# Kernel optimization log

Measured on AMD Instinct MI355X. Metric: run time of the kernel, lower is better.

The kernel has to match this reference:

```python
import jax, jax.numpy as jnp
import numpy as np

NUM_HEADS = 16

def setup_inputs() -> dict:
    key = jax.random.key(0)
    ks = jax.random.split(key, 7)
    B, S, D = 2, 2048, 1024
    X = jax.random.normal(ks[0], (B, S, D), dtype=jnp.float32)
    s = 1.0 / np.sqrt(D)
    Wq = jax.random.normal(ks[1], (D, D), dtype=jnp.float32) * s
    Wk = jax.random.normal(ks[2], (D, D), dtype=jnp.float32) * s
    Wv = jax.random.normal(ks[3], (D, D), dtype=jnp.float32) * s
    Wo = jax.random.normal(ks[4], (D, D), dtype=jnp.float32) * s
    bo = jnp.zeros((D,), dtype=jnp.float32)
    return {"X": X, "Wq": Wq, "Wk": Wk, "Wv": Wv, "Wo": Wo, "bo": bo}

def reference(X, Wq, Wk, Wv, Wo, bo):
    B, S, D = X.shape
    H = NUM_HEADS
    hd = D // H
    # project and split heads -> [B, H, S, hd]
    def split(t):
        return t.reshape(B, S, H, hd).transpose(0, 2, 1, 3)
    q = split(X @ Wq)
    k = split(X @ Wk)
    v = split(X @ Wv)
    scores = jnp.einsum('bhqd,bhkd->bhqk', q, k) / jnp.sqrt(jnp.float32(hd))
    causal = jnp.tril(jnp.ones((S, S), dtype=bool))
    scores = jnp.where(causal, scores, -jnp.inf)
    weights = jax.nn.softmax(scores, axis=-1)  # dropout p=0 -> identity
    ctx = jnp.einsum('bhqk,bhkd->bhqd', weights, v)
    ctx = ctx.transpose(0, 2, 1, 3).reshape(B, S, D)
    return ctx @ Wo + bo
```

## Files before the change

### kernel.cpp

```cpp
#include <hip/hip_runtime.h>


typedef __attribute__((ext_vector_type(8))) short short8;
typedef __attribute__((ext_vector_type(4))) float floatx4;

__device__ inline unsigned short f2bf(float f) {
  unsigned u = __float_as_uint(f);
  unsigned r = (u + 0x7fffu + ((u >> 16) & 1u)) >> 16;
  return (unsigned short)r;
}

__device__ __forceinline__ float fast_exp2(float x) {
#if __has_builtin(__builtin_amdgcn_exp2f)
  return __builtin_amdgcn_exp2f(x);
#else
  float r;
  asm volatile("v_exp_f32_e32 %0, %1" : "=v"(r) : "v"(x));
  return r;
#endif
}

__device__ __forceinline__ void gll16(const unsigned short* g, unsigned short* l) {
  __builtin_amdgcn_global_load_lds(
      (const __attribute__((address_space(1))) unsigned int*)(g),
      (__attribute__((address_space(3))) unsigned int*)(l),
      16, 0, 0);
}

constexpr int B_ = 2, S_ = 2048, D_ = 1024, H_ = 16, HD_ = 64;

__global__ __launch_bounds__(256) void prep_inputs(
    const float* __restrict__ x, unsigned short* __restrict__ xb,
    const float* __restrict__ w0, const float* __restrict__ w1,
    const float* __restrict__ w2, const float* __restrict__ w3,
    unsigned short* __restrict__ wt_base)
{
  if (blockIdx.z == 4) {
    const int tid = threadIdx.y * 32 + threadIdx.x;
    const size_t base =
        ((size_t)(blockIdx.y * 32 + blockIdx.x) * 256 + tid) * 16;
#pragma unroll
    for (int half = 0; half < 2; ++half) {
      const size_t i = base + half * 8;
      float4 a = *(const float4*)(x + i);
      float4 b = *(const float4*)(x + i + 4);
      short8 o;
      o[0] = (short)f2bf(a.x); o[1] = (short)f2bf(a.y);
      o[2] = (short)f2bf(a.z); o[3] = (short)f2bf(a.w);
      o[4] = (short)f2bf(b.x); o[5] = (short)f2bf(b.y);
      o[6] = (short)f2bf(b.z); o[7] = (short)f2bf(b.w);
      *(short8*)(xb + i) = o;
    }
    return;
  }
  const float* src;
  switch (blockIdx.z) {
    case 0: src = w0; break;
    case 1: src = w1; break;
    case 2: src = w2; break;
    default: src = w3; break;
  }
  unsigned short* dst = wt_base + (size_t)blockIdx.z * 1024 * 1024;
  __shared__ unsigned short t[32][33];
  const int bx = blockIdx.x * 32;
  const int by = blockIdx.y * 32;
  const int x_ = threadIdx.x;
  for (int yy = threadIdx.y; yy < 32; yy += 8)
    t[yy][x_] = f2bf(src[(size_t)(by + yy) * 1024 + bx + x_]);
  __syncthreads();
  for (int yy = threadIdx.y; yy < 32; yy += 8)
    dst[(size_t)(bx + yy) * 1024 + by + x_] = t[x_][yy];
}

__global__ __launch_bounds__(256) void transpose_v(
    const unsigned short* __restrict__ Vb, unsigned short* __restrict__ Vt)
{
  __shared__ unsigned short t[32][33];
  const int bh = blockIdx.z;
  const int b = bh >> 4, h = bh & 15;
  const int s0 = blockIdx.x * 32, d0 = blockIdx.y * 32;
  const int x = threadIdx.x;
  for (int yy = threadIdx.y; yy < 32; yy += 8)
    t[yy][x] = Vb[(size_t)(b * 2048 + s0 + yy) * 1024 + h * 64 + d0 + x];
  __syncthreads();
  for (int yy = threadIdx.y; yy < 32; yy += 8)
    Vt[((size_t)bh * 64 + d0 + yy) * 2048 + s0 + x] = t[x][yy];
}

__global__ __launch_bounds__(256) void gemm256_qkv(
    const unsigned short* __restrict__ A,
    const unsigned short* __restrict__ Bt,
    unsigned short* __restrict__ Qo,
    unsigned short* __restrict__ Ko,
    unsigned short* __restrict__ Vo)
{
  __shared__ unsigned short sA[2][128 * 32];
  __shared__ unsigned short sB[2][128 * 32];
  const int K = 1024;
  const int m0 = blockIdx.y * 128;
  const int bn0 = blockIdx.x * 128;

  const int tid = threadIdx.x, wave = tid >> 6, lane = tid & 63;
  const int g = lane >> 4, ml = lane & 15;
  const int wm = wave & 1, wn = wave >> 1;

  const unsigned short* ag0 = A + (size_t)(m0 + (tid >> 2)) * K + (tid & 3) * 8;
  const unsigned short* ag1 = ag0 + (size_t)64 * K;
  const unsigned short* bg0 = Bt + (size_t)(bn0 + (tid >> 2)) * K + (tid & 3) * 8;
  const unsigned short* bg1 = bg0 + (size_t)64 * K;
  const int woff = wave * 512;

  floatx4 acc[4][4];
#pragma unroll
  for (int mt = 0; mt < 4; ++mt)
#pragma unroll
    for (int nt = 0; nt < 4; ++nt) acc[mt][nt] = (floatx4){0.f, 0.f, 0.f, 0.f};

  for (int k0 = 0; k0 < K; k0 += 64) {
    __syncthreads();
#pragma unroll
    for (int t = 0; t < 2; ++t) {
      gll16(ag0 + k0 + t * 32, sA[t] + woff);
      gll16(ag1 + k0 + t * 32, sA[t] + 2048 + woff);
      gll16(bg0 + k0 + t * 32, sB[t] + woff);
      gll16(bg1 + k0 + t * 32, sB[t] + 2048 + woff);
    }
    __syncthreads();
#pragma unroll
    for (int t = 0; t < 2; ++t) {
      short8 af[4], bf[4];
#pragma unroll
      for (int mt = 0; mt < 4; ++mt)
        af[mt] = *(const short8*)(sA[t] + (wm * 64 + mt * 16 + ml) * 32 + g * 8);
#pragma unroll
      for (int nt = 0; nt < 4; ++nt)
        bf[nt] = *(const short8*)(sB[t] + (wn * 64 + nt * 16 + ml) * 32 + g * 8);
#pragma unroll
      for (int mt = 0; mt < 4; ++mt)
#pragma unroll
        for (int nt = 0; nt < 4; ++nt)
          acc[mt][nt] = __builtin_amdgcn_mfma_f32_16x16x32_bf16(
              af[mt], bf[nt], acc[mt][nt], 0, 0, 0);
    }
  }

  const int proj = blockIdx.x >> 3;
  unsigned short* out = (proj == 0) ? Qo : (proj == 1) ? Ko : Vo;
  const int col0 = (blockIdx.x & 7) * 128;
#pragma unroll
  for (int mt = 0; mt < 4; ++mt) {
#pragma unroll
    for (int nt = 0; nt < 4; ++nt) {
      const int col = col0 + wn * 64 + nt * 16 + ml;
#pragma unroll
      for (int r = 0; r < 4; ++r) {
        const int row = m0 + wm * 64 + mt * 16 + g * 4 + r;
        out[(size_t)row * 1024 + col] = f2bf(acc[mt][nt][r]);
      }
    }
  }
}

__global__ __launch_bounds__(256) void gemm_wo64(
    const unsigned short* __restrict__ A,
    const unsigned short* __restrict__ Bt,
    const float* __restrict__ bias,
    float* __restrict__ C)
{
  __shared__ unsigned short sA[4][64 * 32];
  __shared__ unsigned short sB[4][128 * 32];
  const int K = 1024;
  const int m0 = blockIdx.y * 64;
  const int bn0 = blockIdx.x * 128;
  const int tid = threadIdx.x, wave = tid >> 6, lane = tid & 63;
  const int g = lane >> 4, ml = lane & 15;
  const int wm = wave & 1, wn = wave >> 1;

  const unsigned short* ag =
      A + (size_t)(m0 + wave * 16 + (lane >> 2)) * K + (lane & 3) * 8;
  const unsigned short* bg0 = Bt + (size_t)(bn0 + (tid >> 2)) * K + (tid & 3) * 8;
  const unsigned short* bg1 = bg0 + (size_t)64 * K;
  const int woff = wave * 512;

  floatx4 acc[2][4];
#pragma unroll
  for (int mt = 0; mt < 2; ++mt)
#pragma unroll
    for (int nt = 0; nt < 4; ++nt) acc[mt][nt] = (floatx4){0.f, 0.f, 0.f, 0.f};

  for (int k0 = 0; k0 < K; k0 += 128) {
    __syncthreads();
#pragma unroll
    for (int t = 0; t < 4; ++t) {
      gll16(ag + k0 + t * 32, sA[t] + woff);
      gll16(bg0 + k0 + t * 32, sB[t] + woff);
      gll16(bg1 + k0 + t * 32, sB[t] + 2048 + woff);
    }
    __syncthreads();
#pragma unroll
    for (int t = 0; t < 4; ++t) {
      short8 af[2], bf[4];
#pragma unroll
      for (int mt = 0; mt < 2; ++mt)
        af[mt] = *(const short8*)(sA[t] + (wm * 32 + mt * 16 + ml) * 32 + g * 8);
#pragma unroll
      for (int nt = 0; nt < 4; ++nt)
        bf[nt] = *(const short8*)(sB[t] + (wn * 64 + nt * 16 + ml) * 32 + g * 8);
#pragma unroll
      for (int mt = 0; mt < 2; ++mt)
#pragma unroll
        for (int nt = 0; nt < 4; ++nt)
          acc[mt][nt] = __builtin_amdgcn_mfma_f32_16x16x32_bf16(
              af[mt], bf[nt], acc[mt][nt], 0, 0, 0);
    }
  }

#pragma unroll
  for (int mt = 0; mt < 2; ++mt) {
#pragma unroll
    for (int nt = 0; nt < 4; ++nt) {
      const int col = bn0 + wn * 64 + nt * 16 + ml;
      const float badd = bias[col];
#pragma unroll
      for (int r = 0; r < 4; ++r) {
        const int row = m0 + wm * 32 + mt * 16 + g * 4 + r;
        C[(size_t)row * 1024 + col] = acc[mt][nt][r] + badd;
      }
    }
  }
}

constexpr int LDP = 72;
constexpr int KTPB = 3;

__device__ __forceinline__ void attn_tile(
    const short8* aq,
    const unsigned short* sK0, const unsigned short* sK1,
    const unsigned short* sV0, const unsigned short* sV1,
    unsigned short* pw, floatx4* acc, float* l,
    const bool diag, const int qrow0, const int kcol0,
    const int g, const int ml)
{
  const float C1 = 0.18033688f;
  const float C2 = -34.6246810f;

  floatx4 s[4];
#pragma unroll
  for (int nb = 0; nb < 4; ++nb) {
    s[nb] = (floatx4){0.f, 0.f, 0.f, 0.f};
    short8 bk0 = *(const short8*)(sK0 + (nb * 16 + ml) * 32 + g * 8);
    s[nb] = __builtin_amdgcn_mfma_f32_16x16x32_bf16(aq[0], bk0, s[nb], 0, 0, 0);
    short8 bk1 = *(const short8*)(sK1 + (nb * 16 + ml) * 32 + g * 8);
    s[nb] = __builtin_amdgcn_mfma_f32_16x16x32_bf16(aq[1], bk1, s[nb], 0, 0, 0);
  }
#pragma unroll
  for (int r = 0; r < 4; ++r) {
    const int qrow = qrow0 + g * 4 + r;
    float rowsum = 0.f;
#pragma unroll
    for (int nb = 0; nb < 4; ++nb) {
      float wv = fast_exp2(fmaf(s[nb][r], C1, C2));
      if (diag && (kcol0 + nb * 16 + ml > qrow)) wv = 0.f;
      const unsigned bits = __float_as_uint(wv);
      pw[(g * 4 + r) * LDP + nb * 16 + ml] = (unsigned short)(bits >> 16);
      rowsum += __uint_as_float(bits & 0xffff0000u);
    }
    l[r] += rowsum;
  }
#pragma unroll
  for (int st = 0; st < 2; ++st) {
    short8 ap = *(const short8*)(pw + ml * LDP + st * 32 + g * 8);
    const unsigned short* sv = st ? sV1 : sV0;
#pragma unroll
    for (int jd = 0; jd < 4; ++jd) {
      short8 bv = *(const short8*)(sv + (jd * 16 + ml) * 32 + g * 8);
      acc[jd] = __builtin_amdgcn_mfma_f32_16x16x32_bf16(ap, bv, acc[jd], 0, 0, 0);
    }
  }
}

__global__ __launch_bounds__(256) void attn_v10(
    const unsigned short* __restrict__ Q,
    const unsigned short* __restrict__ Kg,
    const unsigned short* __restrict__ Vt,
    unsigned short* __restrict__ CTX)
{
  __shared__ unsigned short sK0[KTPB][64 * 32], sK1[KTPB][64 * 32];
  __shared__ unsigned short sV0[KTPB][64 * 32], sV1[KTPB][64 * 32];
  __shared__ unsigned short sP[4 * 16 * LDP];

  const int bh = blockIdx.y;
  const int b = bh >> 4, h = bh & 15;
  const int p = blockIdx.x;
  const int qbA = p, qbB = 31 - p;
  const int qA0 = qbA * 64, qB0 = qbB * 64;
  const int tid = threadIdx.x, wave = tid >> 6, lane = tid & 63;
  const int g = lane >> 4, ml = lane & 15;

  const size_t headoff = (size_t)b * S_ * D_ + (size_t)h * HD_;
  const size_t vtoff   = (size_t)bh * HD_ * S_;

  short8 aqA[2], aqB[2];
  {
    const unsigned short* qp =
        Q + headoff + (size_t)(qA0 + wave * 16 + ml) * D_ + g * 8;
    aqA[0] = *(const short8*)qp;
    aqA[1] = *(const short8*)(qp + 32);
  }
  {
    const unsigned short* qp =
        Q + headoff + (size_t)(qB0 + wave * 16 + ml) * D_ + g * 8;
    aqB[0] = *(const short8*)qp;
    aqB[1] = *(const short8*)(qp + 32);
  }

  floatx4 accA[4], accB[4];
#pragma unroll
  for (int jd = 0; jd < 4; ++jd) {
    accA[jd] = (floatx4){0.f, 0.f, 0.f, 0.f};
    accB[jd] = (floatx4){0.f, 0.f, 0.f, 0.f};
  }
  float lA[4] = {0.f, 0.f, 0.f, 0.f};
  float lB[4] = {0.f, 0.f, 0.f, 0.f};

  const unsigned short* kgb =
      Kg + headoff + (size_t)(wave * 16 + (lane >> 2)) * D_ + (lane & 3) * 8;
  const unsigned short* vgb =
      Vt + vtoff + (size_t)(wave * 16 + (lane >> 2)) * S_ + (lane & 3) * 8;
  unsigned short* pw = sP + wave * 16 * LDP;
  const int woff = wave * 512;

  const int ntiles = qbB + 1;
  for (int kt0 = 0; kt0 < ntiles; kt0 += KTPB) {
    const int cnt = (ntiles - kt0 < KTPB) ? (ntiles - kt0) : KTPB;
    __syncthreads();
#pragma unroll
    for (int t = 0; t < KTPB; ++t) {
      if (t >= cnt) break;
      const int kt = kt0 + t;
      const size_t ko = (size_t)kt * 64 * D_;
      gll16(kgb + ko,      sK0[t] + woff);
      gll16(kgb + ko + 32, sK1[t] + woff);
      gll16(vgb + kt * 64,      sV0[t] + woff);
      gll16(vgb + kt * 64 + 32, sV1[t] + woff);
    }
    __syncthreads();

#pragma unroll
    for (int t = 0; t < KTPB; ++t) {
      if (t >= cnt) break;
      const int kt = kt0 + t;
      attn_tile(aqB, sK0[t], sK1[t], sV0[t], sV1[t], pw, accB, lB,
                kt == qbB, qB0 + wave * 16, kt * 64, g, ml);
    }
#pragma unroll
    for (int t = 0; t < KTPB; ++t) {
      if (t >= cnt) break;
      const int kt = kt0 + t;
      if (kt <= qbA)
        attn_tile(aqA, sK0[t], sK1[t], sV0[t], sV1[t], pw, accA, lA,
                  kt == qbA, qA0 + wave * 16, kt * 64, g, ml);
    }
  }

#pragma unroll
  for (int r = 0; r < 4; ++r) {
    float la = lA[r];
    la += __shfl_xor(la, 1); la += __shfl_xor(la, 2);
    la += __shfl_xor(la, 4); la += __shfl_xor(la, 8);
    lA[r] = 1.0f / la;
    float lb = lB[r];
    lb += __shfl_xor(lb, 1); lb += __shfl_xor(lb, 2);
    lb += __shfl_xor(lb, 4); lb += __shfl_xor(lb, 8);
    lB[r] = 1.0f / lb;
  }
#pragma unroll
  for (int r = 0; r < 4; ++r) {
    const int rowA = qA0 + wave * 16 + g * 4 + r;
    const int rowB = qB0 + wave * 16 + g * 4 + r;
#pragma unroll
    for (int jd = 0; jd < 4; ++jd) {
      CTX[headoff + (size_t)rowA * D_ + jd * 16 + ml] = f2bf(accA[jd][r] * lA[r]);
      CTX[headoff + (size_t)rowB * D_ + jd * 16 + ml] = f2bf(accB[jd][r] * lB[r]);
    }
  }
}

extern "C" void kernel_launch(void* const* d_in, const int* in_sizes, int n_in,
                              void* d_out, int out_size, void* d_ws, size_t ws_size,
                              hipStream_t stream)
{
  const float* X  = (const float*)d_in[0];
  const float* Wq = (const float*)d_in[1];
  const float* Wk = (const float*)d_in[2];
  const float* Wv = (const float*)d_in[3];
  const float* Wo = (const float*)d_in[4];
  const float* bo = (const float*)d_in[5];

  char* ws = (char*)d_ws;
  const size_t MB = 1024 * 1024;

  unsigned short* Qb  = (unsigned short*)(ws);
  unsigned short* Kb  = (unsigned short*)(ws + 8 * MB);
  unsigned short* Xb  = (unsigned short*)(ws + 16 * MB);
  unsigned short* WT  = (unsigned short*)(ws + 24 * MB);
  unsigned short* WoT = WT + (size_t)3 * 1024 * 1024;
  unsigned short* Vb  = (unsigned short*)d_out;
  unsigned short* Vt  = Xb;

  prep_inputs<<<dim3(32, 32, 5), dim3(32, 8), 0, stream>>>(
      X, Xb, Wq, Wk, Wv, Wo, WT);
  gemm256_qkv<<<dim3(24, 32), 256, 0, stream>>>(Xb, WT, Qb, Kb, Vb);
  transpose_v<<<dim3(64, 2, 32), dim3(32, 8), 0, stream>>>(Vb, Vt);
  attn_v10<<<dim3(16, B_ * H_), 256, 0, stream>>>(Qb, Kb, Vt, Qb);
  gemm_wo64<<<dim3(8, 64), 256, 0, stream>>>(Qb, WoT, bo, (float*)d_out);
}
```

Baseline: 193.6 us.

## Split attention KV tiles across two wave groups and merge partials in LDS

The attention kernel moves to 512 threads. The two groups of four waves each process alternating key tiles for the same query rows, with KTPB reduced to 2, and K and V loads are divided between the groups. At the end, one group writes its partial accumulators and row sums into a shared-memory union buffer and the other group adds them before normalising. The aim is to double the waves per block and improve latency hiding on the causal attention. The cost is an extra reduction step, more barriers, and higher LDS use per block.

Measured after the change: 205.5 us. 1.06x slower.

```diff
diff --git a/kernel.cpp b/kernel.cpp
--- a/kernel.cpp
+++ b/kernel.cpp
@@ -231,7 +231,19 @@
 }
 
 constexpr int LDP = 72;
-constexpr int KTPB = 3;
+constexpr int KTPB = 2;
+
+struct AttnLds {
+  unsigned short k0[KTPB][64 * 32];
+  unsigned short k1[KTPB][64 * 32];
+  unsigned short v0[KTPB][64 * 32];
+  unsigned short v1[KTPB][64 * 32];
+  unsigned short p[8 * 16 * LDP];
+};
+union __align__(16) AttnLdsU {
+  AttnLds t;
+  float comb[4 * 64 * 40];
+};
 
 __device__ __forceinline__ void attn_tile(
     const short8* aq,
@@ -279,22 +291,21 @@
   }
 }
 
-__global__ __launch_bounds__(256) void attn_v10(
+__global__ __launch_bounds__(512) void attn_v11(
     const unsigned short* __restrict__ Q,
     const unsigned short* __restrict__ Kg,
     const unsigned short* __restrict__ Vt,
     unsigned short* __restrict__ CTX)
 {
-  __shared__ unsigned short sK0[KTPB][64 * 32], sK1[KTPB][64 * 32];
-  __shared__ unsigned short sV0[KTPB][64 * 32], sV1[KTPB][64 * 32];
-  __shared__ unsigned short sP[4 * 16 * LDP];
+  __shared__ AttnLdsU lds;
 
   const int bh = blockIdx.y;
   const int b = bh >> 4, h = bh & 15;
   const int p = blockIdx.x;
   const int qbA = p, qbB = 31 - p;
   const int qA0 = qbA * 64, qB0 = qbB * 64;
-  const int tid = threadIdx.x, wave = tid >> 6, lane = tid & 63;
+  const int tid = threadIdx.x, w = tid >> 6, lane = tid & 63;
+  const int slice = w & 3, par = w >> 2;
   const int g = lane >> 4, ml = lane & 15;
 
   const size_t headoff = (size_t)b * S_ * D_ + (size_t)h * HD_;
@@ -303,13 +314,13 @@
   short8 aqA[2], aqB[2];
   {
     const unsigned short* qp =
-        Q + headoff + (size_t)(qA0 + wave * 16 + ml) * D_ + g * 8;
+        Q + headoff + (size_t)(qA0 + slice * 16 + ml) * D_ + g * 8;
     aqA[0] = *(const short8*)qp;
     aqA[1] = *(const short8*)(qp + 32);
   }
   {
     const unsigned short* qp =
-        Q + headoff + (size_t)(qB0 + wave * 16 + ml) * D_ + g * 8;
+        Q + headoff + (size_t)(qB0 + slice * 16 + ml) * D_ + g * 8;
     aqB[0] = *(const short8*)qp;
     aqB[1] = *(const short8*)(qp + 32);
   }
@@ -323,12 +334,13 @@
   float lA[4] = {0.f, 0.f, 0.f, 0.f};
   float lB[4] = {0.f, 0.f, 0.f, 0.f};
 
+  const int sw = slice;
   const unsigned short* kgb =
-      Kg + headoff + (size_t)(wave * 16 + (lane >> 2)) * D_ + (lane & 3) * 8;
+      Kg + headoff + (size_t)(sw * 16 + (lane >> 2)) * D_ + (lane & 3) * 8;
   const unsigned short* vgb =
-      Vt + vtoff + (size_t)(wave * 16 + (lane >> 2)) * S_ + (lane & 3) * 8;
-  unsigned short* pw = sP + wave * 16 * LDP;
-  const int woff = wave * 512;
+      Vt + vtoff + (size_t)(sw * 16 + (lane >> 2)) * S_ + (lane & 3) * 8;
+  unsigned short* pw = lds.t.p + w * 16 * LDP;
+  const int woff = sw * 512;
 
   const int ntiles = qbB + 1;
   for (int kt0 = 0; kt0 < ntiles; kt0 += KTPB) {
@@ -338,28 +350,53 @@
     for (int t = 0; t < KTPB; ++t) {
       if (t >= cnt) break;
       const int kt = kt0 + t;
-      const size_t ko = (size_t)kt * 64 * D_;
-      gll16(kgb + ko,      sK0[t] + woff);
-      gll16(kgb + ko + 32, sK1[t] + woff);
-      gll16(vgb + kt * 64,      sV0[t] + woff);
-      gll16(vgb + kt * 64 + 32, sV1[t] + woff);
-    }
-    __syncthreads();
-
-#pragma unroll
-    for (int t = 0; t < KTPB; ++t) {
-      if (t >= cnt) break;
-      const int kt = kt0 + t;
-      attn_tile(aqB, sK0[t], sK1[t], sV0[t], sV1[t], pw, accB, lB,
-                kt == qbB, qB0 + wave * 16, kt * 64, g, ml);
-    }
-#pragma unroll
-    for (int t = 0; t < KTPB; ++t) {
-      if (t >= cnt) break;
-      const int kt = kt0 + t;
+      if (w < 4) {
+        const size_t ko = (size_t)kt * 64 * D_;
+        gll16(kgb + ko,      lds.t.k0[t] + woff);
+        gll16(kgb + ko + 32, lds.t.k1[t] + woff);
+      } else {
+        gll16(vgb + kt * 64,      lds.t.v0[t] + woff);
+        gll16(vgb + kt * 64 + 32, lds.t.v1[t] + woff);
+      }
+    }
+    __syncthreads();
+
+    if (par < cnt) {
+      const int kt = kt0 + par;
+      attn_tile(aqB, lds.t.k0[par], lds.t.k1[par], lds.t.v0[par], lds.t.v1[par],
+                pw, accB, lB, kt == qbB, qB0 + slice * 16, kt * 64, g, ml);
       if (kt <= qbA)
-        attn_tile(aqA, sK0[t], sK1[t], sV0[t], sV1[t], pw, accA, lA,
-                  kt == qbA, qA0 + wave * 16, kt * 64, g, ml);
+        attn_tile(aqA, lds.t.k0[par], lds.t.k1[par], lds.t.v0[par], lds.t.v1[par],
+                  pw, accA, lA, kt == qbA, qA0 + slice * 16, kt * 64, g, ml);
+    }
+  }
+
+  __syncthreads();
+  {
+    float* slot = lds.comb + (size_t)(slice * 64 + lane) * 40;
+    if (par == 1) {
+#pragma unroll
+      for (int jd = 0; jd < 4; ++jd) {
+        *(floatx4*)(slot + jd * 4) = accA[jd];
+        *(floatx4*)(slot + 20 + jd * 4) = accB[jd];
+      }
+#pragma unroll
+      for (int r = 0; r < 4; ++r) {
+        slot[16 + r] = lA[r];
+        slot[36 + r] = lB[r];
+      }
+    }
+    __syncthreads();
+    if (par == 1) return;
+#pragma unroll
+    for (int jd = 0; jd < 4; ++jd) {
+      accA[jd] += *(const floatx4*)(slot + jd * 4);
+      accB[jd] += *(const floatx4*)(slot + 20 + jd * 4);
+    }
+#pragma unroll
+    for (int r = 0; r < 4; ++r) {
+      lA[r] += slot[16 + r];
+      lB[r] += slot[36 + r];
     }
   }
 
@@ -376,8 +413,8 @@
   }
 #pragma unroll
   for (int r = 0; r < 4; ++r) {
-    const int rowA = qA0 + wave * 16 + g * 4 + r;
-    const int rowB = qB0 + wave * 16 + g * 4 + r;
+    const int rowA = qA0 + slice * 16 + g * 4 + r;
+    const int rowB = qB0 + slice * 16 + g * 4 + r;
 #pragma unroll
     for (int jd = 0; jd < 4; ++jd) {
       CTX[headoff + (size_t)rowA * D_ + jd * 16 + ml] = f2bf(accA[jd][r] * lA[r]);
@@ -412,6 +449,6 @@
       X, Xb, Wq, Wk, Wv, Wo, WT);
   gemm256_qkv<<<dim3(24, 32), 256, 0, stream>>>(Xb, WT, Qb, Kb, Vb);
   transpose_v<<<dim3(64, 2, 32), dim3(32, 8), 0, stream>>>(Vb, Vt);
-  attn_v10<<<dim3(16, B_ * H_), 256, 0, stream>>>(Qb, Kb, Vt, Qb);
+  attn_v11<<<dim3(16, B_ * H_), 512, 0, stream>>>(Qb, Kb, Vt, Qb);
   gemm_wo64<<<dim3(8, 64), 256, 0, stream>>>(Qb, WoT, bo, (float*)d_out);
 }
```
